# Optimization experiments

Measured on AMD Instinct MI355X. Metric: run time of the kernel, lower is better.

Reference implementation:

```python
import jax, jax.numpy as jnp
import numpy as np

M1, M2, M3 = 12, 12, 8
WIDTH = 32


def _spectral_conv(v, wr, wi):
    # v: [B, C, X, Y, T]; wr/wi: [4, Ci, Co, M1, M2, M3]
    B, C, X, Y, T = v.shape
    vft = jnp.fft.rfftn(v, axes=(-3, -2, -1))  # [B,C,X,Y,T//2+1] complex
    w = wr.astype(jnp.complex64) + 1j * wi.astype(jnp.complex64)
    mul = lambda blk, ww: jnp.einsum('bixyz,ioxyz->boxyz', blk, ww)
    out = jnp.zeros((B, wr.shape[2], X, Y, T // 2 + 1), dtype=vft.dtype)
    out = out.at[:, :, :M1, :M2, :M3].set(mul(vft[:, :, :M1, :M2, :M3], w[0]))
    out = out.at[:, :, -M1:, :M2, :M3].set(mul(vft[:, :, -M1:, :M2, :M3], w[1]))
    out = out.at[:, :, :M1, -M2:, :M3].set(mul(vft[:, :, :M1, -M2:, :M3], w[2]))
    out = out.at[:, :, -M1:, -M2:, :M3].set(mul(vft[:, :, -M1:, -M2:, :M3], w[3]))
    return jnp.fft.irfftn(out, s=(X, Y, T), axes=(-3, -2, -1))


def _conv1x1(v, w, b):
    # v: [B,C,X,Y,T]; w: [Co,Ci]; b: [Co]
    return jnp.einsum('bixyz,oi->boxyz', v, w) + b[None, :, None, None, None]


def setup_inputs() -> dict:
    key = jax.random.key(0)
    ks = jax.random.split(key, 24)
    B, X, Y, T = 8, 64, 64, 40
    W = WIDTH
    scale = 1.0 / (W * W)
    d = {}
    d['h'] = jax.random.normal(ks[0], (B, X, Y, T, 2), dtype=jnp.float32)
    d['x'] = jax.random.normal(ks[1], (B, X, Y, T, 3), dtype=jnp.float32)
    d['fc0_w'] = jax.random.normal(ks[2], (5, W), dtype=jnp.float32) * 0.3
    d['fc0_b'] = jnp.zeros((W,), dtype=jnp.float32)
    for i, name in enumerate(['sc0', 'sc1', 'sc3']):
        d[name + '_wr'] = scale * jax.random.uniform(ks[3 + 2 * i], (4, W, W, M1, M2, M3), dtype=jnp.float32)
        d[name + '_wi'] = scale * jax.random.uniform(ks[4 + 2 * i], (4, W, W, M1, M2, M3), dtype=jnp.float32)
    for i, name in enumerate(['w0', 'w1', 'w3']):
        d[name + '_w'] = jax.random.normal(ks[9 + 2 * i], (W, W), dtype=jnp.float32) * (1.0 / np.sqrt(W))
        d[name + '_b'] = jnp.zeros((W,), dtype=jnp.float32)
    d['fc1_w'] = jax.random.normal(ks[15], (W, 64), dtype=jnp.float32) * (1.0 / np.sqrt(W))
    d['fc1_b'] = jnp.zeros((64,), dtype=jnp.float32)
    d['fc2_w'] = jax.random.normal(ks[16], (64, 2), dtype=jnp.float32) * 0.125
    d['fc2_b'] = jnp.zeros((2,), dtype=jnp.float32)
    return d


def reference(h, x, fc0_w, fc0_b, sc0_wr, sc0_wi, sc1_wr, sc1_wi, sc3_wr, sc3_wi,
              w0_w, w0_b, w1_w, w1_b, w3_w, w3_b, fc1_w, fc1_b, fc2_w, fc2_b):
    v = jnp.concatenate((h, x), axis=-1)                 # [B,X,Y,T,5]
    v = v @ fc0_w + fc0_b                                # lift to width
    v = jnp.transpose(v, (0, 4, 1, 2, 3))                # [B,W,X,Y,T]
    v = jax.nn.gelu(_spectral_conv(v, sc0_wr, sc0_wi) + _conv1x1(v, w0_w, w0_b), approximate=False)
    v = jax.nn.gelu(_spectral_conv(v, sc1_wr, sc1_wi) + _conv1x1(v, w1_w, w1_b), approximate=False)
    v = _spectral_conv(v, sc3_wr, sc3_wi) + _conv1x1(v, w3_w, w3_b)
    v = jnp.transpose(v, (0, 2, 3, 4, 1))                # [B,X,Y,T,W]
    v = jax.nn.gelu(v @ fc1_w + fc1_b, approximate=False)
    return v @ fc2_w + fc2_b                             # [B,X,Y,T,2]
```

## Files before the change

kernel.cpp:

```cpp
#include <hip/hip_runtime.h>
#include <math.h>

#define BATCH 8
#define WID   32
#define NX    64
#define NY    64
#define NT    40
#define M1C   12
#define KT    8
#define KXC   24
#define KYC   24
#define NXY   (NX*NY)
#define NXYT  (NXY*NT)
#define NP    (BATCH*NXYT)

#define TWO_PI 6.283185307179586f

static __device__ __forceinline__ float gelu_f(float v){
  return 0.5f*v*(1.0f + erff(v*0.7071067811865476f));
}

static __device__ __forceinline__ void barrier_lds(){
  asm volatile("s_waitcnt lgkmcnt(0)\n\ts_barrier" ::: "memory");
}


__global__ __launch_bounds__(256) void k_fc0(const float* __restrict__ h, const float* __restrict__ x,
                                             const float* __restrict__ w, const float* __restrict__ b,
                                             float* __restrict__ V){
  __shared__ float sw[160], sb[32];
  int tid=threadIdx.x;
  if(tid<160) sw[tid]=w[tid];
  if(tid<32)  sb[tid]=b[tid];
  __syncthreads();
  int pl = tid>>3, q = tid&7;
  int p = blockIdx.x*32 + pl;
  float i0=h[(size_t)p*2], i1=h[(size_t)p*2+1];
  float i2=x[(size_t)p*3], i3=x[(size_t)p*3+1], i4=x[(size_t)p*3+2];
  int c0=q*4;
  float4 o;
  float* po=(float*)&o;
  #pragma unroll
  for(int u=0;u<4;u++){
    int c=c0+u;
    po[u] = sb[c] + i0*sw[c] + i1*sw[32+c] + i2*sw[64+c] + i3*sw[96+c] + i4*sw[128+c];
  }
  ((float4*)V)[(size_t)p*8 + q] = o;
}

__global__ __launch_bounds__(256) void k_fwd_ty(const float* __restrict__ V, float2* __restrict__ F2){
  __shared__ __align__(16) unsigned char smem[55296];
  float*  vt0   = (float*)smem;
  float*  vt1   = (float*)(smem+21504);
  float2* twy   = (float2*)(smem+43008);
  float2* f2out = (float2*)smem;
  int tid = threadIdx.x;
  int b = blockIdx.x >> 6, x = blockIdx.x & 63;
  int c = tid & 31, k = tid >> 5;
  for(int i=tid;i<KYC*NY;i+=256){
    int ky=i>>6, y=i&63;
    int f = ky<M1C ? ky : ky+40;
    float ang = -TWO_PI*(float)((f*y)%NY)/(float)NY;
    twy[i] = make_float2(cosf(ang), sinf(ang));
  }
  float2 twr[20];
  #pragma unroll
  for(int t=0;t<20;t++){
    float ang = -TWO_PI*(float)((k*t)%NT)/(float)NT;
    twr[t] = make_float2(cosf(ang), sinf(ang));
  }
  int toff = (k&1)*20;
  float2 acc[KYC];
  #pragma unroll
  for(int q=0;q<KYC;q++) acc[q]=make_float2(0.f,0.f);
  const float4* src = (const float4*)(V + (size_t)(b*NX+x)*(NY*NT*WID));

  float4 pa[3], pb[3];
  #pragma unroll
  for(int i=0;i<3;i++){
    int s = tid + i*256;
    if(s<640){
      int c4=s&7, t=(s>>3)%20, y=s/160;
      pa[i] = src[y*320 + t*8 + c4];
      pb[i] = src[y*320 + t*8 + c4 + 160];
    }
  }
  #pragma unroll
  for(int i=0;i<3;i++){
    int s = tid + i*256;
    if(s<640){
      int c4=s&7, t=(s>>3)%20, y=s/160;
      float* bse = vt0 + y*1344 + t;
      #pragma unroll
      for(int e=0;e<4;e++){
        float av=((float*)&pa[i])[e], bv=((float*)&pb[i])[e];
        bse[(4*c4+e)*42]      = av+bv;
        bse[(4*c4+e)*42 + 20] = av-bv;
      }
    }
  }
  #pragma unroll
  for(int i=0;i<3;i++){
    int s = tid + i*256;
    if(s<640){
      int c4=s&7, t=(s>>3)%20, y=s/160;
      pa[i] = src[1280 + y*320 + t*8 + c4];
      pb[i] = src[1280 + y*320 + t*8 + c4 + 160];
    }
  }
  __syncthreads();

  #pragma unroll 1
  for(int g=0; g<16; ++g){
    const float* vb = (g&1) ? vt1 : vt0;
    float* vn       = (g&1) ? vt0 : vt1;
    if(g+1<16){
      #pragma unroll
      for(int i=0;i<3;i++){
        int s = tid + i*256;
        if(s<640){
          int c4=s&7, t=(s>>3)%20, y=s/160;
          float* bse = vn + y*1344 + t;
          #pragma unroll
          for(int e=0;e<4;e++){
            float av=((float*)&pa[i])[e], bv=((float*)&pb[i])[e];
            bse[(4*c4+e)*42]      = av+bv;
            bse[(4*c4+e)*42 + 20] = av-bv;
          }
        }
      }
      if(g+2<16){
        const float4* sg = src + (size_t)(g+2)*1280;
        #pragma unroll
        for(int i=0;i<3;i++){
          int s = tid + i*256;
          if(s<640){
            int c4=s&7, t=(s>>3)%20, y=s/160;
            pa[i] = sg[y*320 + t*8 + c4];
            pb[i] = sg[y*320 + t*8 + c4 + 160];
          }
        }
      }
    }
    #pragma unroll
    for(int yl=0; yl<4; yl+=2){
      const float* vp0 = vb + yl*1344 + c*42 + toff;
      const float* vp1 = vp0 + 1344;
      float sr0=0.f,si0=0.f,sr1=0.f,si1=0.f;
      #pragma unroll
      for(int it=0; it<5; it++){
        float2 a0 = *(const float2*)(vp0 + it*4);
        float2 b0 = *(const float2*)(vp0 + it*4 + 2);
        float2 a1 = *(const float2*)(vp1 + it*4);
        float2 b1 = *(const float2*)(vp1 + it*4 + 2);
        float2 w0=twr[it*4], w1=twr[it*4+1], w2=twr[it*4+2], w3=twr[it*4+3];
        sr0 += a0.x*w0.x + a0.y*w1.x + b0.x*w2.x + b0.y*w3.x;
        si0 += a0.x*w0.y + a0.y*w1.y + b0.x*w2.y + b0.y*w3.y;
        sr1 += a1.x*w0.x + a1.y*w1.x + b1.x*w2.x + b1.y*w3.x;
        si1 += a1.x*w0.y + a1.y*w1.y + b1.x*w2.y + b1.y*w3.y;
      }
      int y = g*4 + yl;
      #pragma unroll
      for(int q=0;q<KYC;q++){
        float4 wy = *(const float4*)&twy[q*NY + y];
        acc[q].x += sr0*wy.x - si0*wy.y + sr1*wy.z - si1*wy.w;
        acc[q].y += sr0*wy.y + si0*wy.x + sr1*wy.w + si1*wy.z;
      }
    }
    barrier_lds();
  }
  #pragma unroll
  for(int q=0;q<KYC;q++) f2out[c*193 + q*8 + k] = acc[q];
  __syncthreads();
  for(int i=tid;i<WID*KYC*KT;i+=256){
    int cc=i/192, e=i-cc*192;
    F2[((size_t)(b*WID+cc)*NX + x)*(KYC*KT) + e] = f2out[cc*193 + e];
  }
}

__global__ __launch_bounds__(256) void k_fwd_x(const float2* __restrict__ F2, float2* __restrict__ F3){
  __shared__ float2 tile[NX*KT];
  __shared__ float2 twi[KXC*65];
  int tid=threadIdx.x;
  int bc = blockIdx.x / KYC;
  int ky = blockIdx.x - bc*KYC;
  for(int i=tid;i<NX*KT;i+=256){
    int xx=i/KT, kt=i-xx*KT;
    tile[i] = F2[((size_t)bc*NX + xx)*(KYC*KT) + ky*KT + kt];
  }
  for(int i=tid;i<KXC*NX;i+=256){
    int kx=i/NX, xx=i-kx*NX;
    int f = kx<M1C ? kx : kx+40;
    float ang = -TWO_PI*(float)((f*xx)%NX)/(float)NX;
    twi[kx*65+xx] = make_float2(cosf(ang), sinf(ang));
  }
  __syncthreads();
  for(int item=tid; item<KXC*KT; item+=256){
    int kx=item/KT, kt=item-kx*KT;
    float sr=0.f, si=0.f;
    #pragma unroll 8
    for(int xx=0;xx<NX;xx++){
      float2 a = tile[xx*KT+kt];
      float2 w = twi[kx*65+xx];
      sr += a.x*w.x - a.y*w.y;
      si += a.x*w.y + a.y*w.x;
    }
    F3[(size_t)bc*(KXC*KYC*KT) + kx*(KYC*KT) + ky*KT + kt] = make_float2(sr,si);
  }
}

__global__ __launch_bounds__(256) void k_mix(const float2* __restrict__ F3, const float* __restrict__ wr,
                                             const float* __restrict__ wi, float2* __restrict__ F4){
  __shared__ float2 f3s[BATCH*WID*KT];
  int tid = threadIdx.x;
  int kx = blockIdx.x / KYC, ky = blockIdx.x - kx*KYC;
  int mode0 = blockIdx.x * KT;
  int xp = (kx>=M1C), yp = (ky>=M1C);
  int m1 = kx - M1C*xp, m2 = ky - M1C*yp;
  int blk = xp + 2*yp;
  for(int i=tid;i<1024;i+=256){
    int row=i>>2, q=i&3;
    ((float4*)f3s)[row*4+q] = ((const float4*)(F3 + (size_t)row*4608 + mode0))[q];
  }
  int o = tid>>3, kt = tid&7;
  size_t wbase = (size_t)blk*1179648 + (size_t)o*1152 + m1*96 + m2*8 + kt;
  float wre[WID], wim[WID];
  #pragma unroll
  for(int i=0;i<WID;i++){
    wre[i] = wr[wbase + (size_t)i*36864];
    wim[i] = wi[wbase + (size_t)i*36864];
  }
  __syncthreads();
  #pragma unroll
  for(int b=0;b<BATCH;b++){
    float ar=0.f, ai=0.f;
    #pragma unroll
    for(int i=0;i<WID;i++){
      float2 a = f3s[(b*WID+i)*KT + kt];
      ar += a.x*wre[i] - a.y*wim[i];
      ai += a.x*wim[i] + a.y*wre[i];
    }
    F4[(size_t)(b*WID+o)*4608 + mode0 + kt] = make_float2(ar,ai);
  }
}

__global__ __launch_bounds__(256) void k_inv_x(const float2* __restrict__ F4, float2* __restrict__ F2){
  __shared__ float2 tile[KXC*KT];
  __shared__ float2 twi[NX*25];
  int tid=threadIdx.x;
  int bc = blockIdx.x / KYC, ky = blockIdx.x - (blockIdx.x/KYC)*KYC;
  for(int i=tid;i<KXC*KT;i+=256){
    int kx=i/KT, kt=i-kx*KT;
    tile[i] = F4[(size_t)bc*4608 + kx*(KYC*KT) + ky*KT + kt];
  }
  for(int i=tid;i<NX*KXC;i+=256){
    int xx=i/KXC, kx=i-xx*KXC;
    int f = kx<M1C ? kx : kx+40;
    float ang = TWO_PI*(float)((f*xx)%NX)/(float)NX;
    twi[xx*25+kx] = make_float2(cosf(ang)*(1.0f/64.0f), sinf(ang)*(1.0f/64.0f));
  }
  __syncthreads();
  for(int item=tid; item<NX*KT; item+=256){
    int xx=item/KT, kt=item-xx*KT;
    float sr=0.f, si=0.f;
    #pragma unroll 8
    for(int kx=0;kx<KXC;kx++){
      float2 a = tile[kx*KT+kt];
      float2 w = twi[xx*25+kx];
      sr += a.x*w.x - a.y*w.y;
      si += a.x*w.y + a.y*w.x;
    }
    F2[((size_t)bc*NX + xx)*(KYC*KT) + ky*KT + kt] = make_float2(sr,si);
  }
}

template<bool GELU>
__global__ __launch_bounds__(256) void k_conv(const float2* __restrict__ F2, const float* __restrict__ wcv,
                                              const float* __restrict__ bcv, float* __restrict__ V){
  __shared__ __align__(16) unsigned char smem[34816];
  float*  vtA  = (float*)smem;
  float*  vtB  = (float*)(smem+10240);
  float2* ftc0 = (float2*)(smem+20480);
  float2* ftc1 = (float2*)(smem+24576);
  float2* twy  = (float2*)(smem+28672);
  float2* f2h  = (float2*)smem;

  int tid=threadIdx.x;
  int b  = blockIdx.x >> 7;
  int x  = (blockIdx.x >> 1) & 63;
  int y0 = (blockIdx.x & 1) * 32;
  int cid = tid & 31, ktid = tid >> 5;
  int oid = tid & 31, tg  = tid >> 5;

  float2 fr[KYC];
  #pragma unroll
  for(int half=0; half<2; half++){
    for(int i=tid;i<1536;i+=256){
      int cc=i/96, q=i-cc*96;
      ((float4*)f2h)[i] = *((const float4*)(F2 + ((size_t)(b*WID + half*16 + cc)*NX + x)*(KYC*KT)) + q);
    }
    __syncthreads();
    if((cid>>4) == half){
      const float2* fp = f2h + (cid&15)*192 + ktid;
      #pragma unroll
      for(int ky=0;ky<KYC;ky++) fr[ky] = fp[ky*8];
    }
    __syncthreads();
  }
  {
    float ts = (ktid==0 ? 1.0f : 2.0f) * (1.0f/(float)NT);
    #pragma unroll
    for(int ky=0;ky<KYC;ky++){ fr[ky].x *= ts; fr[ky].y *= ts; }
  }
  float wreg[WID];
  #pragma unroll
  for(int cc=0;cc<WID;cc++) wreg[cc] = wcv[oid*WID + cc];
  float breg = bcv[oid];
  float2 twtg[KT];
  #pragma unroll
  for(int k=0;k<KT;k++){
    float ang = 0.78539816339744831f*(float)((k*tg)&7);
    twtg[k] = make_float2(cosf(ang), sinf(ang));
  }
  for(int i=tid;i<32*KYC;i+=256){
    int yy=i/KYC, ky=i-yy*KYC;
    int f = ky<M1C ? ky : ky+40;
    float ang = TWO_PI*(float)((f*(y0+yy))%NY)/(float)NY;
    twy[i] = make_float2(cosf(ang)*(1.0f/64.0f), sinf(ang)*(1.0f/64.0f));
  }
  float* plane = V + (size_t)((b*NX+x)*NY + y0)*(NT*WID);
  const float4* gp = (const float4*)plane;
  bool has3 = tid < 128;
  {
    float4 p0 = gp[tid], p1 = gp[256+tid];
    float4 p2 = has3 ? gp[512+tid] : make_float4(0,0,0,0);
    ((float4*)vtA)[tid] = p0;
    ((float4*)vtA)[256+tid] = p1;
    if(has3) ((float4*)vtA)[512+tid] = p2;
  }
  float4 rA = gp[640+tid], rB = gp[640+256+tid];
  float4 rC = has3 ? gp[640+512+tid] : make_float4(0,0,0,0);
  __syncthreads();

  constexpr float CJ[KT][5] = {
    {1.f, 1.f,          1.f,          1.f,          1.f         },
    {1.f, 0.98768834f,  0.95105652f,  0.89100652f,  0.80901699f },
    {1.f, 0.95105652f,  0.80901699f,  0.58778525f,  0.30901699f },
    {1.f, 0.89100652f,  0.58778525f,  0.15643447f, -0.30901699f },
    {1.f, 0.80901699f,  0.30901699f, -0.30901699f, -0.80901699f },
    {1.f, 0.70710678f,  0.f,         -0.70710678f, -1.f         },
    {1.f, 0.58778525f, -0.30901699f, -0.95105652f, -0.80901699f },
    {1.f, 0.45399050f, -0.58778525f, -0.98768834f, -0.30901699f },
  };
  constexpr float SJ[KT][5] = {
    {0.f, 0.f,          0.f,          0.f,          0.f         },
    {0.f, 0.15643447f,  0.30901699f,  0.45399050f,  0.58778525f },
    {0.f, 0.30901699f,  0.58778525f,  0.80901699f,  0.95105652f },
    {0.f, 0.45399050f,  0.80901699f,  0.98768834f,  0.95105652f },
    {0.f, 0.58778525f,  0.95105652f,  0.95105652f,  0.58778525f },
    {0.f, 0.70710678f,  1.f,          0.70710678f,  0.f         },
    {0.f, 0.80901699f,  0.95105652f,  0.30901699f, -0.58778525f },
    {0.f, 0.89100652f,  0.80901699f, -0.15643447f, -0.95105652f },
  };

  #pragma unroll 1
  for(int it=0; it<16; ++it){
    float*  vcur = (it&1) ? vtB  : vtA;
    float*  vnxt = (it&1) ? vtA  : vtB;
    float2* fcur = (it&1) ? ftc1 : ftc0;
    int yl = it*2;
    {
      const float2* tw0 = twy + (size_t)yl*KYC;
      const float2* tw1 = tw0 + KYC;
      float sr0=0.f, si0=0.f, sr1=0.f, si1=0.f;
      #pragma unroll
      for(int ky=0;ky<KYC;ky+=2){
        float2 a  = fr[ky];
        float2 b2 = fr[ky+1];
        float4 w0 = *(const float4*)&tw0[ky];
        float4 w1 = *(const float4*)&tw1[ky];
        sr0 += a.x*w0.x - a.y*w0.y + b2.x*w0.z - b2.y*w0.w;
        si0 += a.x*w0.y + a.y*w0.x + b2.x*w0.w + b2.y*w0.z;
        sr1 += a.x*w1.x - a.y*w1.y + b2.x*w1.z - b2.y*w1.w;
        si1 += a.x*w1.y + a.y*w1.x + b2.x*w1.w + b2.y*w1.z;
      }
      fcur[      ktid*32 + cid] = make_float2(sr0,si0);
      fcur[256 + ktid*32 + cid] = make_float2(sr1,si1);
    }
    barrier_lds();
    if(it+1 < 16){
      ((float4*)vnxt)[tid] = rA;
      ((float4*)vnxt)[256+tid] = rB;
      if(has3) ((float4*)vnxt)[512+tid] = rC;
    }
    if(it+2 < 16){
      const float4* q = gp + (size_t)(it+2)*640;
      rA = q[tid]; rB = q[256+tid];
      if(has3) rC = q[512+tid];
    }
    #pragma unroll
    for(int yy=0; yy<2; yy++){
      const float2* fsrc = fcur + yy*256;
      const float*  vb   = vcur + yy*1280;
      float* outp = plane + (size_t)(yl+yy)*(NT*WID);
      float acc[5];
      #pragma unroll
      for(int j=0;j<5;j++) acc[j] = breg;
      #pragma unroll
      for(int k=0;k<KT;k++){
        float2 f = fsrc[k*32 + oid];
        float gx = f.x*twtg[k].x - f.y*twtg[k].y;
        float gy = f.x*twtg[k].y + f.y*twtg[k].x;
        #pragma unroll
        for(int j=0;j<5;j++) acc[j] += gx*CJ[k][j] - gy*SJ[k][j];
      }
      #pragma unroll
      for(int j=0;j<5;j++){
        int t = tg*5 + j;
        float a = acc[j];
        const float* vrow = vb + t*32;
        #pragma unroll
        for(int c4=0;c4<WID;c4+=4){
          float4 vv = *(const float4*)(vrow + c4);
          a += vv.x*wreg[c4] + vv.y*wreg[c4+1] + vv.z*wreg[c4+2] + vv.w*wreg[c4+3];
        }
        outp[t*32 + oid] = GELU ? gelu_f(a) : a;
      }
    }
  }
}

__global__ __launch_bounds__(256) void k_mlp(const float* __restrict__ V, const float* __restrict__ w1,
                                             const float* __restrict__ b1, const float* __restrict__ w2,
                                             const float* __restrict__ b2, float* __restrict__ out){
  __shared__ float sw1t[64*WID];
  __shared__ float sb1[64], sw2[128], sb2[2];
  int tid=threadIdx.x;
  for(int i=tid;i<64*WID;i+=256){ int j=i>>5, c=i&31; sw1t[i]=w1[c*64+j]; }
  if(tid<64) sb1[tid]=b1[tid];
  if(tid<128) sw2[tid]=w2[tid];
  if(tid<2) sb2[tid]=b2[tid];
  __syncthreads();
  size_t p0 = (size_t)blockIdx.x*1024 + (size_t)tid*4;
  float vv[128];
  const float4* vp = (const float4*)(V + p0*WID);
  #pragma unroll
  for(int q=0;q<32;q++) *((float4*)(vv+4*q)) = vp[q];
  float oa[8];
  #pragma unroll
  for(int pt=0;pt<4;pt++){ oa[2*pt]=sb2[0]; oa[2*pt+1]=sb2[1]; }
  #pragma unroll 4
  for(int j=0;j<64;j++){
    float a0=sb1[j], a1=a0, a2=a0, a3=a0;
    const float* wrow = sw1t + j*WID;
    #pragma unroll
    for(int c4=0;c4<WID;c4+=4){
      float4 w = *(const float4*)(wrow + c4);
      a0 += vv[     c4]*w.x + vv[     c4+1]*w.y + vv[     c4+2]*w.z + vv[     c4+3]*w.w;
      a1 += vv[32 + c4]*w.x + vv[32 + c4+1]*w.y + vv[32 + c4+2]*w.z + vv[32 + c4+3]*w.w;
      a2 += vv[64 + c4]*w.x + vv[64 + c4+1]*w.y + vv[64 + c4+2]*w.z + vv[64 + c4+3]*w.w;
      a3 += vv[96 + c4]*w.x + vv[96 + c4+1]*w.y + vv[96 + c4+2]*w.z + vv[96 + c4+3]*w.w;
    }
    a0=gelu_f(a0); a1=gelu_f(a1); a2=gelu_f(a2); a3=gelu_f(a3);
    float u0=sw2[2*j], u1=sw2[2*j+1];
    oa[0]+=a0*u0; oa[1]+=a0*u1; oa[2]+=a1*u0; oa[3]+=a1*u1;
    oa[4]+=a2*u0; oa[5]+=a2*u1; oa[6]+=a3*u0; oa[7]+=a3*u1;
  }
  float4* op = (float4*)(out + p0*2);
  op[0]=make_float4(oa[0],oa[1],oa[2],oa[3]);
  op[1]=make_float4(oa[4],oa[5],oa[6],oa[7]);
}

extern "C" void kernel_launch(void* const* d_in, const int* in_sizes, int n_in,
                              void* d_out, int out_size, void* d_ws, size_t ws_size,
                              hipStream_t stream){
  const float* h     = (const float*)d_in[0];
  const float* x     = (const float*)d_in[1];
  const float* fc0_w = (const float*)d_in[2];
  const float* fc0_b = (const float*)d_in[3];
  const float* scwr[3] = {(const float*)d_in[4], (const float*)d_in[6], (const float*)d_in[8]};
  const float* scwi[3] = {(const float*)d_in[5], (const float*)d_in[7], (const float*)d_in[9]};
  const float* cw[3]   = {(const float*)d_in[10], (const float*)d_in[12], (const float*)d_in[14]};
  const float* cb[3]   = {(const float*)d_in[11], (const float*)d_in[13], (const float*)d_in[15]};
  const float* fc1_w = (const float*)d_in[16];
  const float* fc1_b = (const float*)d_in[17];
  const float* fc2_w = (const float*)d_in[18];
  const float* fc2_b = (const float*)d_in[19];

  const size_t VSZ = (size_t)BATCH*WID*NXYT;
  float*  V  = (float*)d_ws;
  float2* F2 = (float2*)(V + VSZ);
  float2* F4 = F2 + (size_t)BATCH*WID*NX*KYC*KT;
  float2* F3 = (float2*)d_out;

  k_fc0<<<NP/32, 256, 0, stream>>>(h, x, fc0_w, fc0_b, V);
  for(int L=0; L<3; L++){
    k_fwd_ty<<<BATCH*NX, 256, 0, stream>>>(V, F2);
    k_fwd_x<<<(BATCH*WID)*KYC, 256, 0, stream>>>(F2, F3);
    k_mix<<<KXC*KYC, 256, 0, stream>>>(F3, scwr[L], scwi[L], F4);
    k_inv_x<<<(BATCH*WID)*KYC, 256, 0, stream>>>(F4, F2);
    if(L<2) k_conv<true ><<<BATCH*NX*2, 256, 0, stream>>>(F2, cw[L], cb[L], V);
    else    k_conv<false><<<BATCH*NX*2, 256, 0, stream>>>(F2, cw[L], cb[L], V);
  }
  k_mlp<<<NP/1024, 256, 0, stream>>>(V, fc1_w, fc1_b, fc2_w, fc2_b, (float*)d_out);
}
```

Before: 1.402 ms.

## Split forward T/Y DFT across two half-blocks with 512 threads and reduce

Doubles the k_fwd_ty block to 512 threads, with each 256-thread half processing alternating pairs of y rows using its own double-buffered LDS tiles. The two partial accumulators are combined through shared memory at the end. The aim is more waves per block to hide memory and LDS latency, since the grid has only 512 blocks. The cost is an extra reduction pass and possibly lower occupancy, because the 512-thread launch bound limits registers while each thread still holds 24 complex accumulators.

```diff
diff --git a/kernel.cpp b/kernel.cpp
--- a/kernel.cpp
+++ b/kernel.cpp
@@ -48,16 +48,15 @@
   ((float4*)V)[(size_t)p*8 + q] = o;
 }
 
-__global__ __launch_bounds__(256) void k_fwd_ty(const float* __restrict__ V, float2* __restrict__ F2){
+__global__ __launch_bounds__(512) void k_fwd_ty(const float* __restrict__ V, float2* __restrict__ F2){
   __shared__ __align__(16) unsigned char smem[55296];
-  float*  vt0   = (float*)smem;
-  float*  vt1   = (float*)(smem+21504);
   float2* twy   = (float2*)(smem+43008);
   float2* f2out = (float2*)smem;
   int tid = threadIdx.x;
+  int h = tid >> 8, t8 = tid & 255;
   int b = blockIdx.x >> 6, x = blockIdx.x & 63;
-  int c = tid & 31, k = tid >> 5;
-  for(int i=tid;i<KYC*NY;i+=256){
+  int c = t8 & 31, k = t8 >> 5;
+  for(int i=tid;i<KYC*NY;i+=512){
     int ky=i>>6, y=i&63;
     int f = ky<M1C ? ky : ky+40;
     float ang = -TWO_PI*(float)((f*y)%NY)/(float)NY;
@@ -69,97 +68,103 @@
     float ang = -TWO_PI*(float)((k*t)%NT)/(float)NT;
     twr[t] = make_float2(cosf(ang), sinf(ang));
   }
+  float sgn = (k&1) ? -1.0f : 1.0f;
   int toff = (k&1)*20;
   float2 acc[KYC];
   #pragma unroll
   for(int q=0;q<KYC;q++) acc[q]=make_float2(0.f,0.f);
   const float4* src = (const float4*)(V + (size_t)(b*NX+x)*(NY*NT*WID));
-
-  float4 pa[3], pb[3];
-  #pragma unroll
-  for(int i=0;i<3;i++){
-    int s = tid + i*256;
-    if(s<640){
-      int c4=s&7, t=(s>>3)%20, y=s/160;
-      pa[i] = src[y*320 + t*8 + c4];
-      pb[i] = src[y*320 + t*8 + c4 + 160];
-    }
-  }
-  #pragma unroll
-  for(int i=0;i<3;i++){
-    int s = tid + i*256;
-    if(s<640){
-      int c4=s&7, t=(s>>3)%20, y=s/160;
-      float* bse = vt0 + y*1344 + t;
+  float* myb0 = (float*)(smem + h*21504);
+  float* myb1 = myb0 + 2688;
+
+  int s0 = t8;
+  int c40 = s0&7, t0s = (s0>>3)%20, yl0 = s0/160;
+  bool has1 = (t8 < 64);
+  int s1 = t8 + 256;
+  int c41 = s1&7, t1s = (s1>>3)%20, yl1 = s1/160;
+
+  float4 pa0, pb0, pa1, pb1;
+  pa0 = src[(2*h + yl0)*320 + t0s*8 + c40];
+  pb0 = src[(2*h + yl0)*320 + t0s*8 + c40 + 160];
+  if(has1){
+    pa1 = src[(2*h + yl1)*320 + t1s*8 + c41];
+    pb1 = src[(2*h + yl1)*320 + t1s*8 + c41 + 160];
+  }
+  {
+    float* bse = myb0 + yl0*1344 + t0s;
+    #pragma unroll
+    for(int e=0;e<4;e++){
+      float av=((float*)&pa0)[e], bv=((float*)&pb0)[e];
+      bse[(4*c40+e)*42]      = av+bv;
+      bse[(4*c40+e)*42 + 20] = av-bv;
+    }
+    if(has1){
+      float* bs1 = myb0 + yl1*1344 + t1s;
       #pragma unroll
       for(int e=0;e<4;e++){
-        float av=((float*)&pa[i])[e], bv=((float*)&pb[i])[e];
-        bse[(4*c4+e)*42]      = av+bv;
-        bse[(4*c4+e)*42 + 20] = av-bv;
-      }
-    }
-  }
-  #pragma unroll
-  for(int i=0;i<3;i++){
-    int s = tid + i*256;
-    if(s<640){
-      int c4=s&7, t=(s>>3)%20, y=s/160;
-      pa[i] = src[1280 + y*320 + t*8 + c4];
-      pb[i] = src[1280 + y*320 + t*8 + c4 + 160];
-    }
+        float av=((float*)&pa1)[e], bv=((float*)&pb1)[e];
+        bs1[(4*c41+e)*42]      = av+bv;
+        bs1[(4*c41+e)*42 + 20] = av-bv;
+      }
+    }
+  }
+  pa0 = src[(2*(h+2) + yl0)*320 + t0s*8 + c40];
+  pb0 = src[(2*(h+2) + yl0)*320 + t0s*8 + c40 + 160];
+  if(has1){
+    pa1 = src[(2*(h+2) + yl1)*320 + t1s*8 + c41];
+    pb1 = src[(2*(h+2) + yl1)*320 + t1s*8 + c41 + 160];
   }
   __syncthreads();
 
   #pragma unroll 1
-  for(int g=0; g<16; ++g){
-    const float* vb = (g&1) ? vt1 : vt0;
-    float* vn       = (g&1) ? vt0 : vt1;
-    if(g+1<16){
-      #pragma unroll
-      for(int i=0;i<3;i++){
-        int s = tid + i*256;
-        if(s<640){
-          int c4=s&7, t=(s>>3)%20, y=s/160;
-          float* bse = vn + y*1344 + t;
-          #pragma unroll
-          for(int e=0;e<4;e++){
-            float av=((float*)&pa[i])[e], bv=((float*)&pb[i])[e];
-            bse[(4*c4+e)*42]      = av+bv;
-            bse[(4*c4+e)*42 + 20] = av-bv;
-          }
+  for(int it=0; it<16; ++it){
+    int g = 2*it + h;
+    const float* vb = (it&1) ? myb1 : myb0;
+    float*       vn = (it&1) ? myb0 : myb1;
+    if(it+1<16){
+      float* bse = vn + yl0*1344 + t0s;
+      #pragma unroll
+      for(int e=0;e<4;e++){
+        float av=((float*)&pa0)[e], bv=((float*)&pb0)[e];
+        bse[(4*c40+e)*42]      = av+bv;
+        bse[(4*c40+e)*42 + 20] = av-bv;
+      }
+      if(has1){
+        float* bs1 = vn + yl1*1344 + t1s;
+        #pragma unroll
+        for(int e=0;e<4;e++){
+          float av=((float*)&pa1)[e], bv=((float*)&pb1)[e];
+          bs1[(4*c41+e)*42]      = av+bv;
+          bs1[(4*c41+e)*42 + 20] = av-bv;
         }
       }
-      if(g+2<16){
-        const float4* sg = src + (size_t)(g+2)*1280;
-        #pragma unroll
-        for(int i=0;i<3;i++){
-          int s = tid + i*256;
-          if(s<640){
-            int c4=s&7, t=(s>>3)%20, y=s/160;
-            pa[i] = sg[y*320 + t*8 + c4];
-            pb[i] = sg[y*320 + t*8 + c4 + 160];
-          }
+      if(it+2<16){
+        const float4* sg = src + (size_t)(2*(g+4))*320;
+        pa0 = sg[yl0*320 + t0s*8 + c40];
+        pb0 = sg[yl0*320 + t0s*8 + c40 + 160];
+        if(has1){
+          pa1 = sg[yl1*320 + t1s*8 + c41];
+          pb1 = sg[yl1*320 + t1s*8 + c41 + 160];
         }
       }
     }
-    #pragma unroll
-    for(int yl=0; yl<4; yl+=2){
-      const float* vp0 = vb + yl*1344 + c*42 + toff;
+    {
+      const float* vp0 = vb + c*42 + toff;
       const float* vp1 = vp0 + 1344;
       float sr0=0.f,si0=0.f,sr1=0.f,si1=0.f;
       #pragma unroll
-      for(int it=0; it<5; it++){
-        float2 a0 = *(const float2*)(vp0 + it*4);
-        float2 b0 = *(const float2*)(vp0 + it*4 + 2);
-        float2 a1 = *(const float2*)(vp1 + it*4);
-        float2 b1 = *(const float2*)(vp1 + it*4 + 2);
-        float2 w0=twr[it*4], w1=twr[it*4+1], w2=twr[it*4+2], w3=twr[it*4+3];
+      for(int i5=0; i5<5; i5++){
+        float2 a0 = *(const float2*)(vp0 + i5*4);
+        float2 b0 = *(const float2*)(vp0 + i5*4 + 2);
+        float2 a1 = *(const float2*)(vp1 + i5*4);
+        float2 b1 = *(const float2*)(vp1 + i5*4 + 2);
+        float2 w0=twr[i5*4], w1=twr[i5*4+1], w2=twr[i5*4+2], w3=twr[i5*4+3];
         sr0 += a0.x*w0.x + a0.y*w1.x + b0.x*w2.x + b0.y*w3.x;
         si0 += a0.x*w0.y + a0.y*w1.y + b0.x*w2.y + b0.y*w3.y;
         sr1 += a1.x*w0.x + a1.y*w1.x + b1.x*w2.x + b1.y*w3.x;
         si1 += a1.x*w0.y + a1.y*w1.y + b1.x*w2.y + b1.y*w3.y;
       }
-      int y = g*4 + yl;
+      int y = 2*g;
       #pragma unroll
       for(int q=0;q<KYC;q++){
         float4 wy = *(const float4*)&twy[q*NY + y];
@@ -169,10 +174,21 @@
     }
     barrier_lds();
   }
-  #pragma unroll
-  for(int q=0;q<KYC;q++) f2out[c*193 + q*8 + k] = acc[q];
-  __syncthreads();
-  for(int i=tid;i<WID*KYC*KT;i+=256){
+  (void)sgn;
+  if(h==0){
+    #pragma unroll
+    for(int q=0;q<KYC;q++) f2out[c*193 + q*8 + k] = acc[q];
+  }
+  __syncthreads();
+  if(h==1){
+    #pragma unroll
+    for(int q=0;q<KYC;q++){
+      float2 v = f2out[c*193 + q*8 + k];
+      f2out[c*193 + q*8 + k] = make_float2(v.x+acc[q].x, v.y+acc[q].y);
+    }
+  }
+  __syncthreads();
+  for(int i=tid;i<WID*KYC*KT;i+=512){
     int cc=i/192, e=i-cc*192;
     F2[((size_t)(b*WID+cc)*NX + x)*(KYC*KT) + e] = f2out[cc*193 + e];
   }
@@ -495,7 +511,7 @@
 
   k_fc0<<<NP/32, 256, 0, stream>>>(h, x, fc0_w, fc0_b, V);
   for(int L=0; L<3; L++){
-    k_fwd_ty<<<BATCH*NX, 256, 0, stream>>>(V, F2);
+    k_fwd_ty<<<BATCH*NX, 512, 0, stream>>>(V, F2);
     k_fwd_x<<<(BATCH*WID)*KYC, 256, 0, stream>>>(F2, F3);
     k_mix<<<KXC*KYC, 256, 0, stream>>>(F3, scwr[L], scwi[L], F4);
     k_inv_x<<<(BATCH*WID)*KYC, 256, 0, stream>>>(F4, F2);
```

After: 1.393 ms. Within noise of the previous version (-0.7%).
